# Kernel tuning notes

Measured on AMD Instinct MI355X. Metric: run time of the kernel, lower is better.

Reference implementation:

```python
import jax, jax.numpy as jnp
import numpy as np
import math

B, S, DM, H = 2, 2048, 1024, 16
HD = DM // H  # head_dim = 64


def setup_inputs() -> dict:
    key = jax.random.key(0)
    ks = jax.random.split(key, 7)
    mk = lambda k, shp, s=1.0: jax.random.normal(k, shp, dtype=jnp.float32) * s
    return {
        "q": mk(ks[0], (B, S, DM)),
        "k": mk(ks[1], (B, S, DM)),
        "v": mk(ks[2], (B, S, DM)),
        "wq": mk(ks[3], (DM, DM), 0.02),
        "wk": mk(ks[4], (DM, DM), 0.02),
        "wv": mk(ks[5], (DM, DM), 0.02),
        "wo": mk(ks[6], (DM, DM), 0.02),
    }


def reference(q, k, v, wq, wk, wv, wo):
    bsz, seqlen, _ = q.shape
    # bias-free linear projections: y = x @ W.T (torch nn.Linear layout [out,in])
    def proj(x, w):
        y = jnp.einsum('bsd,ed->bse', x, w)
        return y.reshape(bsz, seqlen, H, HD).transpose(0, 2, 1, 3)  # (B,H,S,HD)
    xq, xk, xv = proj(q, wq), proj(k, wk), proj(v, wv)
    scores = jnp.einsum('bhqd,bhkd->bhqk', xq, xk) / math.sqrt(HD)  # (B,H,S,S)
    # causal mask: -inf above the diagonal
    causal = jnp.tril(jnp.ones((seqlen, seqlen), dtype=bool))
    scores = jnp.where(causal[None, None], scores, -jnp.inf)
    probs = jax.nn.softmax(scores.astype(jnp.float32), axis=-1).astype(xq.dtype)
    # dropout p=0.0 -> identity in eval / p=0 config
    out = jnp.einsum('bhqk,bhkd->bhqd', probs, xv)  # (B,H,S,HD)
    out = out.transpose(0, 2, 1, 3).reshape(bsz, seqlen, DM)
    return jnp.einsum('bsd,ed->bse', out, wo)
```

## Files before the change

kernel.cpp:

```cpp
#include <hip/hip_runtime.h>
#include <hip/hip_bf16.h>
#include <stdint.h>

#define NB 2
#define NS 2048
#define NDM 1024
#define NH 16
#define NHD 64
#define NTOK (NB * NS)

typedef __bf16 bf16x8 __attribute__((ext_vector_type(8)));
typedef float f32x4 __attribute__((ext_vector_type(4)));
typedef uint16_t u16x8 __attribute__((ext_vector_type(8)));

static __device__ __forceinline__ uint16_t f2bf(float f) {
  __bf16 b = (__bf16)f;
  union { __bf16 b; uint16_t u; } x; x.b = b;
  return x.u;
}

static __device__ __forceinline__ u16x8 cvt8(float4 a, float4 b) {
  u16x8 v;
  v[0] = f2bf(a.x); v[1] = f2bf(a.y); v[2] = f2bf(a.z); v[3] = f2bf(a.w);
  v[4] = f2bf(b.x); v[5] = f2bf(b.y); v[6] = f2bf(b.z); v[7] = f2bf(b.w);
  return v;
}

static __device__ __forceinline__ void gload_lds16(const void* g, void* l) {
  __builtin_amdgcn_global_load_lds(
      (const __attribute__((address_space(1))) void*)g,
      (__attribute__((address_space(3))) void*)l, 16, 0, 0);
}

__global__ __launch_bounds__(256) void cvt_w(
    const float* __restrict__ w0, const float* __restrict__ w1,
    const float* __restrict__ w2, const float* __restrict__ w3,
    uint16_t* __restrict__ o0, uint16_t* __restrict__ o1,
    uint16_t* __restrict__ o2, uint16_t* __restrict__ o3) {
  int y = blockIdx.y;
  const float* src = (y == 0) ? w0 : (y == 1) ? w1 : (y == 2) ? w2 : w3;
  uint16_t* dst = (y == 0) ? o0 : (y == 1) ? o1 : (y == 2) ? o2 : o3;
  int i = ((int)blockIdx.x * 256 + (int)threadIdx.x) * 8;
  float4 a = *(const float4*)(src + i);
  float4 b = *(const float4*)(src + i + 4);
  *(u16x8*)&dst[i] = cvt8(a, b);
}

__global__ __launch_bounds__(256) void cvt_x(
    const float* __restrict__ x0, const float* __restrict__ x1,
    const float* __restrict__ x2, uint16_t* __restrict__ o0,
    uint16_t* __restrict__ o1, uint16_t* __restrict__ o2) {
  int y = blockIdx.y;
  const float* src = (y == 0) ? x0 : (y == 1) ? x1 : x2;
  uint16_t* dst = (y == 0) ? o0 : (y == 1) ? o1 : o2;
  int i = ((int)blockIdx.x * 256 + (int)threadIdx.x) * 8;
  float4 a = *(const float4*)(src + i);
  float4 b = *(const float4*)(src + i + 4);
  *(u16x8*)&dst[i] = cvt8(a, b);
}

__global__ __launch_bounds__(256) void proj_gemm(
    const uint16_t* __restrict__ xbq, const uint16_t* __restrict__ xbk,
    const uint16_t* __restrict__ xbv, const uint16_t* __restrict__ wqb,
    const uint16_t* __restrict__ wkb, const uint16_t* __restrict__ wvb,
    uint16_t* __restrict__ XQ, uint16_t* __restrict__ XK,
    uint16_t* __restrict__ XVT) {
  __shared__ uint16_t SM[2][2][128][64];
  int z = blockIdx.z;
  const uint16_t* A = (z == 0) ? xbq : (z == 1) ? xbk : xbv;
  const uint16_t* W = (z == 0) ? wqb : (z == 1) ? wkb : wvb;
  int m0 = blockIdx.x * 128, n0 = blockIdx.y * 128;
  int tid = threadIdx.x;
  int lane = tid & 63, w = tid >> 6;
  int g = lane >> 4, r16 = lane & 15;
  int wm = w >> 1, wn = w & 1;
  int bce = ((lane & 7) ^ ((lane >> 3) & 7)) * 8;
  int brlane = lane >> 3;

  f32x4 acc[4][4] = {};

  #pragma unroll
  for (int i = 0; i < 4; ++i) {
    int row = w * 32 + i * 8;
    gload_lds16(A + (size_t)(m0 + row + brlane) * NDM + bce, &SM[0][0][row][0]);
    gload_lds16(W + (size_t)(n0 + row + brlane) * NDM + bce, &SM[0][1][row][0]);
  }
  __syncthreads();

  for (int t = 0; t < 16; ++t) {
    int cur = t & 1, nxt = cur ^ 1;
    if (t < 15) {
      int k1 = (t + 1) * 64;
      #pragma unroll
      for (int i = 0; i < 4; ++i) {
        int row = w * 32 + i * 8;
        gload_lds16(A + (size_t)(m0 + row + brlane) * NDM + k1 + bce,
                    &SM[nxt][0][row][0]);
        gload_lds16(W + (size_t)(n0 + row + brlane) * NDM + k1 + bce,
                    &SM[nxt][1][row][0]);
      }
    }

    #pragma unroll
    for (int kc = 0; kc < 2; ++kc) {
      bf16x8 af[4], bf[4];
      #pragma unroll
      for (int i = 0; i < 4; ++i) {
        int gran = (kc * 4 + g) ^ (r16 & 7);
        af[i] = *(const bf16x8*)&SM[cur][0][wm * 64 + i * 16 + r16][gran * 8];
        bf[i] = *(const bf16x8*)&SM[cur][1][wn * 64 + i * 16 + r16][gran * 8];
      }
      #pragma unroll
      for (int mi = 0; mi < 4; ++mi)
        #pragma unroll
        for (int ni = 0; ni < 4; ++ni)
          acc[mi][ni] = __builtin_amdgcn_mfma_f32_16x16x32_bf16(
              af[mi], bf[ni], acc[mi][ni], 0, 0, 0);
    }
    __syncthreads();
  }

  if (z == 2) {
    uint16_t* T = &SM[0][0][0][0];
    #pragma unroll
    for (int mi = 0; mi < 4; ++mi) {
      #pragma unroll
      for (int ni = 0; ni < 4; ++ni) {
        int tr = wn * 64 + ni * 16 + r16;
        int tc = wm * 64 + mi * 16 + g * 4;
        int gran = tc >> 3, sub = g & 1;
        f32x4 a = acc[mi][ni];
        ushort4 pk;
        pk.x = f2bf(a[0]); pk.y = f2bf(a[1]);
        pk.z = f2bf(a[2]); pk.w = f2bf(a[3]);
        *(ushort4*)(T + tr * 128 + ((gran ^ (tr & 7)) << 3) + (sub << 2)) = pk;
      }
    }
    __syncthreads();
    #pragma unroll
    for (int it = 0; it < 8; ++it) {
      int row = it * 16 + (tid >> 4);
      int grn = tid & 15;
      u16x8 vv = *(const u16x8*)(T + row * 128 + ((grn ^ (row & 7)) << 3));
      *(u16x8*)&XVT[(size_t)(n0 + row) * NTOK + m0 + grn * 8] = vv;
    }
  } else {
    float scale = (z == 0) ? 0.125f * 1.44269504088896340736f : 1.0f;
    uint16_t* Y = (z == 0) ? XQ : XK;
    #pragma unroll
    for (int mi = 0; mi < 4; ++mi) {
      #pragma unroll
      for (int ni = 0; ni < 4; ++ni) {
        int m = m0 + wm * 64 + mi * 16 + g * 4;
        int n = n0 + wn * 64 + ni * 16 + r16;
        f32x4 a = acc[mi][ni];
        #pragma unroll
        for (int j = 0; j < 4; ++j)
          Y[(size_t)(m + j) * NDM + n] = f2bf(a[j] * scale);
      }
    }
  }
}

__global__ __launch_bounds__(256) void attn_kernel(
    const uint16_t* __restrict__ XQ, const uint16_t* __restrict__ XK,
    const uint16_t* __restrict__ XVT, uint16_t* __restrict__ AO) {
  __shared__ uint16_t Klds[64][72];
  __shared__ uint16_t Vlds[64][72];
  __shared__ uint16_t Plds[4][16][72];

  int tid = threadIdx.x;
  int lane = tid & 63;
  int w = tid >> 6;
  int g = lane >> 4, r16 = lane & 15;
  int srow = tid >> 2;
  int scol = (tid & 3) * 16;

  for (int which = 0; which < 2; ++which) {
    int item = (which == 0) ? (int)blockIdx.x : (1023 - (int)blockIdx.x);
    int qc = 31 - (item >> 5);
    int bh = item & 31;
    int b = bh >> 4, h = bh & 15;
    int q0 = qc * 64;
    int q0w = q0 + w * 16;
    int T = qc + 1;

    const uint16_t* qb =
        XQ + (size_t)(b * NS + q0w + r16) * NDM + h * NHD + g * 8;
    bf16x8 qf0 = *(const bf16x8*)qb;
    bf16x8 qf1 = *(const bf16x8*)(qb + 32);

    f32x4 oacc[4] = {};
    float mrow = -1e30f, lsum = 0.f;

    const uint16_t* kbase =
        XK + (size_t)(b * NS + srow) * NDM + h * NHD + scol;
    const uint16_t* vbase =
        XVT + (size_t)(h * NHD + srow) * NTOK + b * NS + scol;

    u16x8 kr0 = *(const u16x8*)(kbase);
    u16x8 kr1 = *(const u16x8*)(kbase + 8);
    u16x8 vr0 = *(const u16x8*)(vbase);
    u16x8 vr1 = *(const u16x8*)(vbase + 8);

    for (int t = 0; t < T; ++t) {
      int kv0 = t * 64;
      __syncthreads();
      *(u16x8*)&Klds[srow][scol]     = kr0;
      *(u16x8*)&Klds[srow][scol + 8] = kr1;
      *(u16x8*)&Vlds[srow][scol]     = vr0;
      *(u16x8*)&Vlds[srow][scol + 8] = vr1;
      __syncthreads();
      if (t + 1 < T) {
        const uint16_t* kp = kbase + (size_t)(t + 1) * 64 * NDM;
        const uint16_t* vp = vbase + (t + 1) * 64;
        kr0 = *(const u16x8*)(kp);
        kr1 = *(const u16x8*)(kp + 8);
        vr0 = *(const u16x8*)(vp);
        vr1 = *(const u16x8*)(vp + 8);
      }

      f32x4 sc[4];
      __builtin_amdgcn_s_setprio(1);
      #pragma unroll
      for (int t4 = 0; t4 < 4; ++t4) {
        bf16x8 kf0 = *(const bf16x8*)&Klds[t4 * 16 + r16][g * 8];
        bf16x8 kf1 = *(const bf16x8*)&Klds[t4 * 16 + r16][32 + g * 8];
        f32x4 x = __builtin_amdgcn_mfma_f32_16x16x32_bf16(
            kf0, qf0, (f32x4){0.f, 0.f, 0.f, 0.f}, 0, 0, 0);
        x = __builtin_amdgcn_mfma_f32_16x16x32_bf16(kf1, qf1, x, 0, 0, 0);
        sc[t4] = x;
      }
      __builtin_amdgcn_s_setprio(0);

      #pragma unroll
      for (int t4 = 0; t4 < 4; ++t4) {
        if (kv0 + t4 * 16 + 15 > q0w) {
          #pragma unroll
          for (int j = 0; j < 4; ++j)
            if (kv0 + t4 * 16 + g * 4 + j > q0w + r16) sc[t4][j] = -1e30f;
        }
      }

      float m16 = fmaxf(
          fmaxf(fmaxf(fmaxf(sc[0][0], sc[0][1]), fmaxf(sc[0][2], sc[0][3])),
                fmaxf(fmaxf(sc[1][0], sc[1][1]), fmaxf(sc[1][2], sc[1][3]))),
          fmaxf(fmaxf(fmaxf(sc[2][0], sc[2][1]), fmaxf(sc[2][2], sc[2][3])),
                fmaxf(fmaxf(sc[3][0], sc[3][1]), fmaxf(sc[3][2], sc[3][3]))));
      m16 = fmaxf(m16, __shfl_xor(m16, 16));
      m16 = fmaxf(m16, __shfl_xor(m16, 32));

      if (!__all(m16 <= mrow + 8.0f)) {
        float mnew = fmaxf(mrow, m16);
        float sf = __builtin_amdgcn_exp2f(mrow - mnew);
        mrow = mnew;
        lsum *= sf;
        #pragma unroll
        for (int j = 0; j < 4; ++j) {
          float sfj = __shfl(sf, g * 4 + j);
          #pragma unroll
          for (int dt = 0; dt < 4; ++dt) oacc[dt][j] *= sfj;
        }
      }

      #pragma unroll
      for (int t4 = 0; t4 < 4; ++t4) {
        float p0 = __builtin_amdgcn_exp2f(sc[t4][0] - mrow);
        float p1 = __builtin_amdgcn_exp2f(sc[t4][1] - mrow);
        float p2 = __builtin_amdgcn_exp2f(sc[t4][2] - mrow);
        float p3 = __builtin_amdgcn_exp2f(sc[t4][3] - mrow);
        lsum += (p0 + p1) + (p2 + p3);
        ushort4 pk;
        pk.x = f2bf(p0); pk.y = f2bf(p1); pk.z = f2bf(p2); pk.w = f2bf(p3);
        *(ushort4*)&Plds[w][r16][t4 * 16 + g * 4] = pk;
      }

      bf16x8 pa0 = *(const bf16x8*)&Plds[w][r16][g * 8];
      bf16x8 pa1 = *(const bf16x8*)&Plds[w][r16][32 + g * 8];
      __builtin_amdgcn_s_setprio(1);
      #pragma unroll
      for (int dt = 0; dt < 4; ++dt) {
        bf16x8 vf0 = *(const bf16x8*)&Vlds[dt * 16 + r16][g * 8];
        bf16x8 vf1 = *(const bf16x8*)&Vlds[dt * 16 + r16][32 + g * 8];
        oacc[dt] = __builtin_amdgcn_mfma_f32_16x16x32_bf16(pa0, vf0, oacc[dt], 0, 0, 0);
        oacc[dt] = __builtin_amdgcn_mfma_f32_16x16x32_bf16(pa1, vf1, oacc[dt], 0, 0, 0);
      }
      __builtin_amdgcn_s_setprio(0);
    }

    float l2 = lsum + __shfl_xor(lsum, 16);
    float ltot = l2 + __shfl_xor(l2, 32);
    #pragma unroll
    for (int j = 0; j < 4; ++j) {
      float lt = __shfl(ltot, g * 4 + j);
      float inv = 1.0f / lt;
      size_t ro = (size_t)(b * NS + q0 + w * 16 + g * 4 + j) * NDM + h * NHD;
      #pragma unroll
      for (int dt = 0; dt < 4; ++dt)
        AO[ro + dt * 16 + r16] = f2bf(oacc[dt][j] * inv);
    }
  }
}

__global__ __launch_bounds__(256) void out_gemm(
    const uint16_t* __restrict__ AO, const uint16_t* __restrict__ wob,
    float* __restrict__ out) {
  __shared__ uint16_t As[2][128][64];
  __shared__ uint16_t Bs[2][128][64];
  int m0 = blockIdx.x * 128, n0 = blockIdx.y * 128;
  int tid = threadIdx.x;
  int lane = tid & 63, w = tid >> 6;
  int g = lane >> 4, r16 = lane & 15;
  int wm = w >> 1, wn = w & 1;
  int bce = ((lane & 7) ^ ((lane >> 3) & 7)) * 8;
  int brlane = lane >> 3;

  f32x4 acc[4][4] = {};

  #pragma unroll
  for (int i = 0; i < 4; ++i) {
    int row = w * 32 + i * 8;
    gload_lds16(AO + (size_t)(m0 + row + brlane) * NDM + bce, &As[0][row][0]);
    gload_lds16(wob + (size_t)(n0 + row + brlane) * NDM + bce, &Bs[0][row][0]);
  }
  __syncthreads();

  for (int t = 0; t < 16; ++t) {
    int cur = t & 1, nxt = cur ^ 1;
    if (t < 15) {
      int k1 = (t + 1) * 64;
      #pragma unroll
      for (int i = 0; i < 4; ++i) {
        int row = w * 32 + i * 8;
        gload_lds16(AO + (size_t)(m0 + row + brlane) * NDM + k1 + bce,
                    &As[nxt][row][0]);
        gload_lds16(wob + (size_t)(n0 + row + brlane) * NDM + k1 + bce,
                    &Bs[nxt][row][0]);
      }
    }

    #pragma unroll
    for (int kc = 0; kc < 2; ++kc) {
      bf16x8 af[4], bf[4];
      #pragma unroll
      for (int i = 0; i < 4; ++i) {
        int gran = (kc * 4 + g) ^ (r16 & 7);
        af[i] = *(const bf16x8*)&As[cur][wm * 64 + i * 16 + r16][gran * 8];
        bf[i] = *(const bf16x8*)&Bs[cur][wn * 64 + i * 16 + r16][gran * 8];
      }
      #pragma unroll
      for (int mi = 0; mi < 4; ++mi)
        #pragma unroll
        for (int ni = 0; ni < 4; ++ni)
          acc[mi][ni] = __builtin_amdgcn_mfma_f32_16x16x32_bf16(
              af[mi], bf[ni], acc[mi][ni], 0, 0, 0);
    }
    __syncthreads();
  }

  #pragma unroll
  for (int mi = 0; mi < 4; ++mi) {
    #pragma unroll
    for (int ni = 0; ni < 4; ++ni) {
      int m = m0 + wm * 64 + mi * 16 + g * 4;
      int n = n0 + wn * 64 + ni * 16 + r16;
      #pragma unroll
      for (int j = 0; j < 4; ++j)
        out[(size_t)(m + j) * NDM + n] = acc[mi][ni][j];
    }
  }
}

extern "C" void kernel_launch(void* const* d_in, const int* in_sizes, int n_in,
                              void* d_out, int out_size, void* d_ws,
                              size_t ws_size, hipStream_t stream) {
  const float* q  = (const float*)d_in[0];
  const float* k  = (const float*)d_in[1];
  const float* v  = (const float*)d_in[2];
  const float* wq = (const float*)d_in[3];
  const float* wk = (const float*)d_in[4];
  const float* wv = (const float*)d_in[5];
  const float* wo = (const float*)d_in[6];

  const size_t XN = (size_t)NTOK * NDM;
  const size_t WN = (size_t)NDM * NDM;
  uint16_t* XQ  = (uint16_t*)d_ws;
  uint16_t* XK  = XQ + XN;
  uint16_t* XVT = XK + XN;
  uint16_t* WQB = XVT + XN;
  uint16_t* WKB = WQB + WN;
  uint16_t* WVB = WKB + WN;
  uint16_t* WOB = WVB + WN;
  uint16_t* XBQ = WOB + WN;
  uint16_t* XBK = XBQ + XN;
  uint16_t* XBV = XBK + XN;
  uint16_t* AO  = XBQ;

  cvt_w<<<dim3(WN / (256 * 8), 4), 256, 0, stream>>>(
      wq, wk, wv, wo, WQB, WKB, WVB, WOB);
  cvt_x<<<dim3(XN / (256 * 8), 3), 256, 0, stream>>>(
      q, k, v, XBQ, XBK, XBV);
  proj_gemm<<<dim3(NTOK / 128, NDM / 128, 3), 256, 0, stream>>>(
      XBQ, XBK, XBV, WQB, WKB, WVB, XQ, XK, XVT);
  attn_kernel<<<dim3(512), 256, 0, stream>>>(XQ, XK, XVT, AO);
  out_gemm<<<dim3(NTOK / 128, NDM / 128), 256, 0, stream>>>(
      AO, WOB, (float*)d_out);
}
```

Before: 117.9 us.

## Split attention into 32-row query tiles with 128-thread blocks, one item each

Attention blocks now handle 32 query rows with two waves instead of 64 rows with four waves, launching 2048 single-item blocks ordered longest-first instead of 512 blocks that each paired a long and a short causal item. This aims for finer-grained load balancing and more resident blocks across the CUs. In exchange, each K/V tile staged in LDS is reused by fewer query rows, roughly doubling K/V global reads, and each thread loads twice as much per tile.

```diff
diff --git a/kernel.cpp b/kernel.cpp
--- a/kernel.cpp
+++ b/kernel.cpp
@@ -162,143 +162,143 @@
   }
 }
 
-__global__ __launch_bounds__(256) void attn_kernel(
+__global__ __launch_bounds__(128) void attn_kernel(
     const uint16_t* __restrict__ XQ, const uint16_t* __restrict__ XK,
     const uint16_t* __restrict__ XVT, uint16_t* __restrict__ AO) {
   __shared__ uint16_t Klds[64][72];
   __shared__ uint16_t Vlds[64][72];
-  __shared__ uint16_t Plds[4][16][72];
+  __shared__ uint16_t Plds[2][16][72];
 
   int tid = threadIdx.x;
   int lane = tid & 63;
   int w = tid >> 6;
   int g = lane >> 4, r16 = lane & 15;
-  int srow = tid >> 2;
-  int scol = (tid & 3) * 16;
-
-  for (int which = 0; which < 2; ++which) {
-    int item = (which == 0) ? (int)blockIdx.x : (1023 - (int)blockIdx.x);
-    int qc = 31 - (item >> 5);
-    int bh = item & 31;
-    int b = bh >> 4, h = bh & 15;
-    int q0 = qc * 64;
-    int q0w = q0 + w * 16;
-    int T = qc + 1;
-
-    const uint16_t* qb =
-        XQ + (size_t)(b * NS + q0w + r16) * NDM + h * NHD + g * 8;
-    bf16x8 qf0 = *(const bf16x8*)qb;
-    bf16x8 qf1 = *(const bf16x8*)(qb + 32);
-
-    f32x4 oacc[4] = {};
-    float mrow = -1e30f, lsum = 0.f;
-
-    const uint16_t* kbase =
-        XK + (size_t)(b * NS + srow) * NDM + h * NHD + scol;
-    const uint16_t* vbase =
-        XVT + (size_t)(h * NHD + srow) * NTOK + b * NS + scol;
-
-    u16x8 kr0 = *(const u16x8*)(kbase);
-    u16x8 kr1 = *(const u16x8*)(kbase + 8);
-    u16x8 vr0 = *(const u16x8*)(vbase);
-    u16x8 vr1 = *(const u16x8*)(vbase + 8);
-
-    for (int t = 0; t < T; ++t) {
-      int kv0 = t * 64;
-      __syncthreads();
-      *(u16x8*)&Klds[srow][scol]     = kr0;
-      *(u16x8*)&Klds[srow][scol + 8] = kr1;
-      *(u16x8*)&Vlds[srow][scol]     = vr0;
-      *(u16x8*)&Vlds[srow][scol + 8] = vr1;
-      __syncthreads();
-      if (t + 1 < T) {
-        const uint16_t* kp = kbase + (size_t)(t + 1) * 64 * NDM;
-        const uint16_t* vp = vbase + (t + 1) * 64;
-        kr0 = *(const u16x8*)(kp);
-        kr1 = *(const u16x8*)(kp + 8);
-        vr0 = *(const u16x8*)(vp);
-        vr1 = *(const u16x8*)(vp + 8);
-      }
-
-      f32x4 sc[4];
-      __builtin_amdgcn_s_setprio(1);
-      #pragma unroll
-      for (int t4 = 0; t4 < 4; ++t4) {
-        bf16x8 kf0 = *(const bf16x8*)&Klds[t4 * 16 + r16][g * 8];
-        bf16x8 kf1 = *(const bf16x8*)&Klds[t4 * 16 + r16][32 + g * 8];
-        f32x4 x = __builtin_amdgcn_mfma_f32_16x16x32_bf16(
-            kf0, qf0, (f32x4){0.f, 0.f, 0.f, 0.f}, 0, 0, 0);
-        x = __builtin_amdgcn_mfma_f32_16x16x32_bf16(kf1, qf1, x, 0, 0, 0);
-        sc[t4] = x;
-      }
-      __builtin_amdgcn_s_setprio(0);
-
-      #pragma unroll
-      for (int t4 = 0; t4 < 4; ++t4) {
-        if (kv0 + t4 * 16 + 15 > q0w) {
-          #pragma unroll
-          for (int j = 0; j < 4; ++j)
-            if (kv0 + t4 * 16 + g * 4 + j > q0w + r16) sc[t4][j] = -1e30f;
-        }
-      }
-
-      float m16 = fmaxf(
-          fmaxf(fmaxf(fmaxf(sc[0][0], sc[0][1]), fmaxf(sc[0][2], sc[0][3])),
-                fmaxf(fmaxf(sc[1][0], sc[1][1]), fmaxf(sc[1][2], sc[1][3]))),
-          fmaxf(fmaxf(fmaxf(sc[2][0], sc[2][1]), fmaxf(sc[2][2], sc[2][3])),
-                fmaxf(fmaxf(sc[3][0], sc[3][1]), fmaxf(sc[3][2], sc[3][3]))));
-      m16 = fmaxf(m16, __shfl_xor(m16, 16));
-      m16 = fmaxf(m16, __shfl_xor(m16, 32));
-
-      if (!__all(m16 <= mrow + 8.0f)) {
-        float mnew = fmaxf(mrow, m16);
-        float sf = __builtin_amdgcn_exp2f(mrow - mnew);
-        mrow = mnew;
-        lsum *= sf;
+  int srow = tid >> 1;
+  int scol = (tid & 1) * 32;
+
+  int item = (int)blockIdx.x;
+  int qc = 63 - (item >> 5);
+  int bh = item & 31;
+  int b = bh >> 4, h = bh & 15;
+  int q0 = qc * 32;
+  int q0w = q0 + w * 16;
+  int T = (qc >> 1) + 1;
+
+  const uint16_t* qb =
+      XQ + (size_t)(b * NS + q0w + r16) * NDM + h * NHD + g * 8;
+  bf16x8 qf0 = *(const bf16x8*)qb;
+  bf16x8 qf1 = *(const bf16x8*)(qb + 32);
+
+  f32x4 oacc[4] = {};
+  float mrow = -1e30f, lsum = 0.f;
+
+  const uint16_t* kbase = XK + (size_t)(b * NS + srow) * NDM + h * NHD + scol;
+  const uint16_t* vbase = XVT + (size_t)(h * NHD + srow) * NTOK + b * NS + scol;
+
+  u16x8 kr[4], vr[4];
+  #pragma unroll
+  for (int i = 0; i < 4; ++i) {
+    kr[i] = *(const u16x8*)(kbase + i * 8);
+    vr[i] = *(const u16x8*)(vbase + i * 8);
+  }
+
+  for (int t = 0; t < T; ++t) {
+    int kv0 = t * 64;
+    __syncthreads();
+    #pragma unroll
+    for (int i = 0; i < 4; ++i) {
+      *(u16x8*)&Klds[srow][scol + i * 8] = kr[i];
+      *(u16x8*)&Vlds[srow][scol + i * 8] = vr[i];
+    }
+    __syncthreads();
+    if (t + 1 < T) {
+      const uint16_t* kp = kbase + (size_t)(t + 1) * 64 * NDM;
+      const uint16_t* vp = vbase + (t + 1) * 64;
+      #pragma unroll
+      for (int i = 0; i < 4; ++i) {
+        kr[i] = *(const u16x8*)(kp + i * 8);
+        vr[i] = *(const u16x8*)(vp + i * 8);
+      }
+    }
+
+    f32x4 sc[4];
+    __builtin_amdgcn_s_setprio(1);
+    #pragma unroll
+    for (int t4 = 0; t4 < 4; ++t4) {
+      bf16x8 kf0 = *(const bf16x8*)&Klds[t4 * 16 + r16][g * 8];
+      bf16x8 kf1 = *(const bf16x8*)&Klds[t4 * 16 + r16][32 + g * 8];
+      f32x4 x = __builtin_amdgcn_mfma_f32_16x16x32_bf16(
+          kf0, qf0, (f32x4){0.f, 0.f, 0.f, 0.f}, 0, 0, 0);
+      x = __builtin_amdgcn_mfma_f32_16x16x32_bf16(kf1, qf1, x, 0, 0, 0);
+      sc[t4] = x;
+    }
+    __builtin_amdgcn_s_setprio(0);
+
+    #pragma unroll
+    for (int t4 = 0; t4 < 4; ++t4) {
+      if (kv0 + t4 * 16 + 15 > q0w) {
         #pragma unroll
-        for (int j = 0; j < 4; ++j) {
-          float sfj = __shfl(sf, g * 4 + j);
-          #pragma unroll
-          for (int dt = 0; dt < 4; ++dt) oacc[dt][j] *= sfj;
-        }
-      }
-
-      #pragma unroll
-      for (int t4 = 0; t4 < 4; ++t4) {
-        float p0 = __builtin_amdgcn_exp2f(sc[t4][0] - mrow);
-        float p1 = __builtin_amdgcn_exp2f(sc[t4][1] - mrow);
-        float p2 = __builtin_amdgcn_exp2f(sc[t4][2] - mrow);
-        float p3 = __builtin_amdgcn_exp2f(sc[t4][3] - mrow);
-        lsum += (p0 + p1) + (p2 + p3);
-        ushort4 pk;
-        pk.x = f2bf(p0); pk.y = f2bf(p1); pk.z = f2bf(p2); pk.w = f2bf(p3);
-        *(ushort4*)&Plds[w][r16][t4 * 16 + g * 4] = pk;
-      }
-
-      bf16x8 pa0 = *(const bf16x8*)&Plds[w][r16][g * 8];
-      bf16x8 pa1 = *(const bf16x8*)&Plds[w][r16][32 + g * 8];
-      __builtin_amdgcn_s_setprio(1);
-      #pragma unroll
-      for (int dt = 0; dt < 4; ++dt) {
-        bf16x8 vf0 = *(const bf16x8*)&Vlds[dt * 16 + r16][g * 8];
-        bf16x8 vf1 = *(const bf16x8*)&Vlds[dt * 16 + r16][32 + g * 8];
-        oacc[dt] = __builtin_amdgcn_mfma_f32_16x16x32_bf16(pa0, vf0, oacc[dt], 0, 0, 0);
-        oacc[dt] = __builtin_amdgcn_mfma_f32_16x16x32_bf16(pa1, vf1, oacc[dt], 0, 0, 0);
-      }
-      __builtin_amdgcn_s_setprio(0);
-    }
-
-    float l2 = lsum + __shfl_xor(lsum, 16);
-    float ltot = l2 + __shfl_xor(l2, 32);
-    #pragma unroll
-    for (int j = 0; j < 4; ++j) {
-      float lt = __shfl(ltot, g * 4 + j);
-      float inv = 1.0f / lt;
-      size_t ro = (size_t)(b * NS + q0 + w * 16 + g * 4 + j) * NDM + h * NHD;
-      #pragma unroll
-      for (int dt = 0; dt < 4; ++dt)
-        AO[ro + dt * 16 + r16] = f2bf(oacc[dt][j] * inv);
-    }
+        for (int j = 0; j < 4; ++j)
+          if (kv0 + t4 * 16 + g * 4 + j > q0w + r16) sc[t4][j] = -1e30f;
+      }
+    }
+
+    float m16 = fmaxf(
+        fmaxf(fmaxf(fmaxf(sc[0][0], sc[0][1]), fmaxf(sc[0][2], sc[0][3])),
+              fmaxf(fmaxf(sc[1][0], sc[1][1]), fmaxf(sc[1][2], sc[1][3]))),
+        fmaxf(fmaxf(fmaxf(sc[2][0], sc[2][1]), fmaxf(sc[2][2], sc[2][3])),
+              fmaxf(fmaxf(sc[3][0], sc[3][1]), fmaxf(sc[3][2], sc[3][3]))));
+    m16 = fmaxf(m16, __shfl_xor(m16, 16));
+    m16 = fmaxf(m16, __shfl_xor(m16, 32));
+
+    if (!__all(m16 <= mrow + 8.0f)) {
+      float mnew = fmaxf(mrow, m16);
+      float sf = __builtin_amdgcn_exp2f(mrow - mnew);
+      mrow = mnew;
+      lsum *= sf;
+      #pragma unroll
+      for (int j = 0; j < 4; ++j) {
+        float sfj = __shfl(sf, g * 4 + j);
+        #pragma unroll
+        for (int dt = 0; dt < 4; ++dt) oacc[dt][j] *= sfj;
+      }
+    }
+
+    #pragma unroll
+    for (int t4 = 0; t4 < 4; ++t4) {
+      float p0 = __builtin_amdgcn_exp2f(sc[t4][0] - mrow);
+      float p1 = __builtin_amdgcn_exp2f(sc[t4][1] - mrow);
+      float p2 = __builtin_amdgcn_exp2f(sc[t4][2] - mrow);
+      float p3 = __builtin_amdgcn_exp2f(sc[t4][3] - mrow);
+      lsum += (p0 + p1) + (p2 + p3);
+      ushort4 pk;
+      pk.x = f2bf(p0); pk.y = f2bf(p1); pk.z = f2bf(p2); pk.w = f2bf(p3);
+      *(ushort4*)&Plds[w][r16][t4 * 16 + g * 4] = pk;
+    }
+
+    bf16x8 pa0 = *(const bf16x8*)&Plds[w][r16][g * 8];
+    bf16x8 pa1 = *(const bf16x8*)&Plds[w][r16][32 + g * 8];
+    __builtin_amdgcn_s_setprio(1);
+    #pragma unroll
+    for (int dt = 0; dt < 4; ++dt) {
+      bf16x8 vf0 = *(const bf16x8*)&Vlds[dt * 16 + r16][g * 8];
+      bf16x8 vf1 = *(const bf16x8*)&Vlds[dt * 16 + r16][32 + g * 8];
+      oacc[dt] = __builtin_amdgcn_mfma_f32_16x16x32_bf16(pa0, vf0, oacc[dt], 0, 0, 0);
+      oacc[dt] = __builtin_amdgcn_mfma_f32_16x16x32_bf16(pa1, vf1, oacc[dt], 0, 0, 0);
+    }
+    __builtin_amdgcn_s_setprio(0);
+  }
+
+  float l2 = lsum + __shfl_xor(lsum, 16);
+  float ltot = l2 + __shfl_xor(l2, 32);
+  #pragma unroll
+  for (int j = 0; j < 4; ++j) {
+    float lt = __shfl(ltot, g * 4 + j);
+    float inv = 1.0f / lt;
+    size_t ro = (size_t)(b * NS + q0 + w * 16 + g * 4 + j) * NDM + h * NHD;
+    #pragma unroll
+    for (int dt = 0; dt < 4; ++dt)
+      AO[ro + dt * 16 + r16] = f2bf(oacc[dt][j] * inv);
   }
 }
 
@@ -402,7 +402,7 @@
       q, k, v, XBQ, XBK, XBV);
   proj_gemm<<<dim3(NTOK / 128, NDM / 128, 3), 256, 0, stream>>>(
       XBQ, XBK, XBV, WQB, WKB, WVB, XQ, XK, XVT);
-  attn_kernel<<<dim3(512), 256, 0, stream>>>(XQ, XK, XVT, AO);
+  attn_kernel<<<dim3(2048), 128, 0, stream>>>(XQ, XK, XVT, AO);
   out_gemm<<<dim3(NTOK / 128, NDM / 128), 256, 0, stream>>>(
       AO, WOB, (float*)d_out);
 }
```

New measurement: 118.6 us. About the same (+0.6%).
